# Performance work log

Measured on AMD Instinct MI355X. Metric: run time of the kernel, lower is better.

## Reference

```python
import jax, jax.numpy as jnp
import numpy as np

NUM_HEADS = 8
EPS = 1e-12  # tf.nn.l2_normalize epsilon


def _l2_normalize(t):
    # tf.nn.l2_normalize: x * rsqrt(max(sum(x^2), eps)) along last axis
    sq = jnp.sum(t * t, axis=-1, keepdims=True)
    return t * jax.lax.rsqrt(jnp.maximum(sq, EPS))


def setup_inputs() -> dict:
    key = jax.random.key(0)
    ks = jax.random.split(key, 4)
    B, N, C = 8, 4096, 512
    x = jax.random.normal(ks[0], (B, N, C), dtype=jnp.float32)
    w_qkv = jax.random.normal(ks[1], (C, 3 * C), dtype=jnp.float32) * (C ** -0.5)
    b_qkv = jnp.zeros((3 * C,), dtype=jnp.float32)
    w_proj = jax.random.normal(ks[2], (C, C), dtype=jnp.float32) * (C ** -0.5)
    b_proj = jnp.zeros((C,), dtype=jnp.float32)
    return {"x": x, "w_qkv": w_qkv, "b_qkv": b_qkv, "w_proj": w_proj, "b_proj": b_proj}


def reference(x, w_qkv, b_qkv, w_proj, b_proj):
    B, N, C = x.shape
    h = NUM_HEADS
    d = C // h
    scale = d ** -0.5
    qkv = x @ w_qkv + b_qkv                        # [B,N,3C]
    qkv = qkv.reshape(B, N, 3, h, d)
    qkv = jnp.transpose(qkv, (2, 0, 3, 1, 4))      # [3,B,h,N,d]
    q, k, v = qkv[0], qkv[1], qkv[2]
    q = _l2_normalize(q) * scale
    k = _l2_normalize(k)
    # channel-wise attention: q^T k over tokens -> [B,h,d,d]
    attn = jnp.einsum('bhnd,bhne->bhde', q, k)
    attn = jax.nn.softmax(attn, axis=-1)
    out = jnp.einsum('bhnd,bhde->bhne', v, attn)   # [B,h,N,d]
    out = jnp.transpose(out, (0, 2, 1, 3)).reshape(B, N, C)
    out = out @ w_proj + b_proj
    return out
```

## Files before the change

kernel.cpp:

```cpp
#include <hip/hip_runtime.h>
#include <stdint.h>

#define NB 8
#define NN 4096
#define NC 512
#define NH 8

typedef __bf16 bf16x8 __attribute__((ext_vector_type(8)));
typedef float floatx4 __attribute__((ext_vector_type(4)));

__device__ __forceinline__ unsigned short f2bf(float f) {
  union { float f; unsigned u; } v; v.f = f;
  return (unsigned short)((v.u + 0x7fffu + ((v.u >> 16) & 1u)) >> 16);
}
__device__ __forceinline__ float bf2f(unsigned short s) {
  union { unsigned u; float f; } v; v.u = ((unsigned)s) << 16;
  return v.f;
}
__device__ __forceinline__ float2 bfp2f(unsigned u) {
  union { unsigned x; float f; } lo, hi;
  lo.x = u << 16; hi.x = u & 0xffff0000u;
  return make_float2(lo.f, hi.f);
}

__device__ __forceinline__ void async_ld16(void* lds, const void* g) {
  auto* gp = (const __attribute__((address_space(1))) unsigned int*)(uintptr_t)g;
  auto* lp = (__attribute__((address_space(3))) unsigned int*)(uintptr_t)lds;
  __builtin_amdgcn_global_load_lds(gp, lp, 16, 0, 0);
}

__global__ __launch_bounds__(256) void k_convert(const float* __restrict__ src,
                                                 unsigned short* __restrict__ dst, int n) {
  int i = (blockIdx.x * 256 + threadIdx.x) * 4;
  if (i >= n) return;
  float4 v = *(const float4*)(src + i);
  ushort4 o;
  o.x = f2bf(v.x); o.y = f2bf(v.y); o.z = f2bf(v.z); o.w = f2bf(v.w);
  *(ushort4*)(dst + i) = o;
}

__global__ __launch_bounds__(256) void k_transpose_cvt(const float* __restrict__ w,
                                                       unsigned short* __restrict__ wt) {
  __shared__ float tile[64][65];
  int nn0 = blockIdx.x * 64, kk0 = blockIdx.y * 64;
  int t = threadIdx.x;
#pragma unroll
  for (int i = 0; i < 16; i++) {
    int id = t + i * 256;
    int r = id >> 6, c = id & 63;
    tile[c][r] = w[(size_t)(kk0 + r) * 1536 + nn0 + c];
  }
  __syncthreads();
#pragma unroll
  for (int i = 0; i < 16; i++) {
    int id = t + i * 256;
    int rn = id >> 6, ck = id & 63;
    wt[(size_t)(nn0 + rn) * 512 + kk0 + ck] = f2bf(tile[rn][ck]);
  }
}

__global__ __launch_bounds__(256) void k_gemm_qkv(const unsigned short* __restrict__ A,
                                                  const unsigned short* __restrict__ Bt,
                                                  const float* __restrict__ bias,
                                                  unsigned short* __restrict__ Cq) {
  const int K = 512, LDA = 512, LDB = 512, LDC = 1536;
  int m0 = blockIdx.x * 128, n0 = blockIdx.y * 128;
  int tid = threadIdx.x;
  int lane = tid & 63, w = tid >> 6;
  int wm = (w & 1) * 64, wn = (w >> 1) * 64;
  int quad = lane >> 4, rr = lane & 15;
  int r8 = lane >> 3, cg = lane & 7;
  int cgs = cg ^ r8;
  const int swz = rr & 7;

  __shared__ __align__(16) unsigned short Als[128][64];
  __shared__ __align__(16) unsigned short Bls[128][64];

  floatx4 acc[4][4];
#pragma unroll
  for (int i = 0; i < 4; i++)
#pragma unroll
    for (int j = 0; j < 4; j++) acc[i][j] = (floatx4){0.f, 0.f, 0.f, 0.f};

  for (int k0 = 0; k0 < K; k0 += 64) {
#pragma unroll
    for (int i = 0; i < 4; i++) {
      int row = i * 32 + w * 8 + r8;
      async_ld16(&Als[i * 32 + w * 8][0], A + (size_t)(m0 + row) * LDA + k0 + cgs * 8);
      async_ld16(&Bls[i * 32 + w * 8][0], Bt + (size_t)(n0 + row) * LDB + k0 + cgs * 8);
    }
    __syncthreads();
#pragma unroll
    for (int kk = 0; kk < 64; kk += 32) {
      int gb = kk >> 3;
      bf16x8 af[4], bfr[4];
#pragma unroll
      for (int mi = 0; mi < 4; mi++)
        af[mi] = *(const bf16x8*)&Als[wm + mi * 16 + rr][(((gb + quad) ^ swz)) * 8];
#pragma unroll
      for (int ni = 0; ni < 4; ni++)
        bfr[ni] = *(const bf16x8*)&Bls[wn + ni * 16 + rr][(((gb + quad) ^ swz)) * 8];
#pragma unroll
      for (int mi = 0; mi < 4; mi++)
#pragma unroll
        for (int ni = 0; ni < 4; ni++)
          acc[mi][ni] = __builtin_amdgcn_mfma_f32_16x16x32_bf16(af[mi], bfr[ni], acc[mi][ni], 0, 0, 0);
    }
    __syncthreads();
  }
#pragma unroll
  for (int ni = 0; ni < 4; ni++) {
    int col = n0 + wn + ni * 16 + rr;
    float bv = bias[col];
#pragma unroll
    for (int mi = 0; mi < 4; mi++) {
      int rbase = m0 + wm + mi * 16 + quad * 4;
#pragma unroll
      for (int r = 0; r < 4; r++)
        Cq[(size_t)(rbase + r) * LDC + col] = f2bf(acc[mi][ni][r] + bv);
    }
  }
}

__global__ __launch_bounds__(256) void k_attn(const unsigned short* __restrict__ QKV,
                                              float* __restrict__ logits_p) {
  int chunk = blockIdx.x, hh = blockIdx.y, b = blockIdx.z;
  int tid = threadIdx.x, w = tid >> 6, l = tid & 63;
  int quad = l >> 4, rr = l & 15;

  __shared__ __align__(16) unsigned char smem[65536];
  unsigned short* qT = (unsigned short*)smem + w * 5120;
  unsigned short* kT = qT + 2560;
  float* ps = (float*)smem;

  floatx4 acc[4][4];
#pragma unroll
  for (int i = 0; i < 4; i++)
#pragma unroll
    for (int j = 0; j < 4; j++) acc[i][j] = (floatx4){0.f, 0.f, 0.f, 0.f};

  int tok8 = l >> 3;
  int seg = l & 7;
  int sw = seg & 3;

  for (int s = 0; s < 4; s++) {
    int nbase = chunk * 512 + w * 128 + s * 32;
#pragma unroll
    for (int c = 0; c < 4; c++) {
      int n = nbase + c * 8 + tok8;
      const unsigned short* p = QKV + (size_t)(b * 4096 + n) * 1536 + hh * 64 + seg * 8;
      uint4 vq = *(const uint4*)p;
      uint4 vk = *(const uint4*)(p + 512);
      unsigned uq[4] = {vq.x, vq.y, vq.z, vq.w};
      unsigned uk[4] = {vk.x, vk.y, vk.z, vk.w};
      float qf[8], kf[8], sq = 0.f, sk = 0.f;
#pragma unroll
      for (int e = 0; e < 4; e++) {
        float2 f = bfp2f(uq[e]); qf[2 * e] = f.x; qf[2 * e + 1] = f.y; sq += f.x * f.x + f.y * f.y;
        float2 g = bfp2f(uk[e]); kf[2 * e] = g.x; kf[2 * e + 1] = g.y; sk += g.x * g.x + g.y * g.y;
      }
      sq += __shfl_xor(sq, 1); sq += __shfl_xor(sq, 2); sq += __shfl_xor(sq, 4);
      sk += __shfl_xor(sk, 1); sk += __shfl_xor(sk, 2); sk += __shfl_xor(sk, 4);
      float scq = 0.125f * rsqrtf(fmaxf(sq, 1e-12f));
      float sck = rsqrtf(fmaxf(sk, 1e-12f));
      int col = ((c ^ sw) << 3) + tok8;
#pragma unroll
      for (int j = 0; j < 8; j++) {
        int dim = seg * 8 + j;
        qT[dim * 40 + col] = f2bf(qf[j] * scq);
        kT[dim * 40 + col] = f2bf(kf[j] * sck);
      }
    }
    bf16x8 af[4], bfr[4];
#pragma unroll
    for (int mi = 0; mi < 4; mi++) {
      int s3 = (mi * 2 + (rr >> 3)) & 3;
      int off = (mi * 16 + rr) * 40 + ((quad ^ s3) << 3);
      af[mi] = *(const bf16x8*)(qT + off);
      bfr[mi] = *(const bf16x8*)(kT + off);
    }
#pragma unroll
    for (int mi = 0; mi < 4; mi++)
#pragma unroll
      for (int ni = 0; ni < 4; ni++)
        acc[mi][ni] = __builtin_amdgcn_mfma_f32_16x16x32_bf16(af[mi], bfr[ni], acc[mi][ni], 0, 0, 0);
  }

  __syncthreads();
#pragma unroll
  for (int mi = 0; mi < 4; mi++)
#pragma unroll
    for (int ni = 0; ni < 4; ni++)
#pragma unroll
      for (int r = 0; r < 4; r++) {
        int d = mi * 16 + quad * 4 + r, e = ni * 16 + rr;
        ps[w * 4096 + d * 64 + e] = acc[mi][ni][r];
      }
  __syncthreads();
  float* outp = logits_p + ((size_t)(b * 8 + hh) * 8 + chunk) * 4096;
  for (int i = tid; i < 4096; i += 256)
    outp[i] = ps[i] + ps[4096 + i] + ps[8192 + i] + ps[12288 + i];
}

__global__ __launch_bounds__(256) void k_softmax_m(const float* __restrict__ logits_p,
                                                   const float* __restrict__ wproj,
                                                   unsigned short* __restrict__ Mt) {
  int cc = blockIdx.x, hh = blockIdx.y, b = blockIdx.z;
  int t = threadIdx.x;
  __shared__ float ls[64][64];
  __shared__ float red[64][4];
  __shared__ float inv[64];
  const float* lp = logits_p + (size_t)((b * 8 + hh) * 8) * 4096;
#pragma unroll
  for (int i = 0; i < 16; i++) {
    int id = t + i * 256;
    float s = 0.f;
#pragma unroll
    for (int c = 0; c < 8; c++) s += lp[c * 4096 + id];
    ls[id >> 6][id & 63] = s;
  }
  __syncthreads();
  int row = t >> 2, part = t & 3;
  float mx = -1e30f;
#pragma unroll
  for (int j = 0; j < 16; j++) mx = fmaxf(mx, ls[row][part * 16 + j]);
  red[row][part] = mx;
  __syncthreads();
  if (part == 0) inv[row] = fmaxf(fmaxf(red[row][0], red[row][1]), fmaxf(red[row][2], red[row][3]));
  __syncthreads();
  float rm = inv[row];
  float s = 0.f;
#pragma unroll
  for (int j = 0; j < 16; j++) {
    float e = __expf(ls[row][part * 16 + j] - rm);
    ls[row][part * 16 + j] = e;
    s += e;
  }
  red[row][part] = s;
  __syncthreads();
  if (part == 0) inv[row] = 1.0f / (red[row][0] + red[row][1] + red[row][2] + red[row][3]);
  __syncthreads();

  int cout = cc * 128 + (t & 127);
  int half = t >> 7;
  float wreg[64];
#pragma unroll
  for (int ee = 0; ee < 64; ee++) wreg[ee] = wproj[(size_t)(hh * 64 + ee) * 512 + cout];
  unsigned short ob[32];
#pragma unroll
  for (int d2 = 0; d2 < 32; d2++) {
    int dd = half * 32 + d2;
    float a = 0.f;
#pragma unroll
    for (int e4 = 0; e4 < 16; e4++) {
      float4 p4 = *(const float4*)&ls[dd][e4 * 4];
      a += p4.x * wreg[e4 * 4] + p4.y * wreg[e4 * 4 + 1] + p4.z * wreg[e4 * 4 + 2] + p4.w * wreg[e4 * 4 + 3];
    }
    ob[d2] = f2bf(a * inv[dd]);
  }
  uint4* dst = (uint4*)(Mt + ((size_t)(b * 512 + cout)) * 512 + hh * 64 + half * 32);
#pragma unroll
  for (int i = 0; i < 4; i++) dst[i] = ((const uint4*)ob)[i];
}

__global__ __launch_bounds__(256) void k_gemm_out(const unsigned short* __restrict__ QKV,
                                                  const unsigned short* __restrict__ MtAll,
                                                  const float* __restrict__ bias,
                                                  float* __restrict__ Out) {
  const int K = 512, LDA = 1536, LDB = 512, LDC = 512;
  int b = blockIdx.x >> 5;
  int m0 = (blockIdx.x & 31) * 128;
  int n0 = blockIdx.y * 128;
  const unsigned short* A = QKV + (size_t)b * NN * 1536 + 1024;
  const unsigned short* Bt = MtAll + (size_t)b * 512 * 512;
  int tid = threadIdx.x;
  int lane = tid & 63, w = tid >> 6;
  int wm = (w & 1) * 64, wn = (w >> 1) * 64;
  int quad = lane >> 4, rr = lane & 15;
  int r8 = lane >> 3, cg = lane & 7;
  int cgs = cg ^ r8;
  const int swz = rr & 7;

  __shared__ __align__(16) unsigned short Als[128][64];
  __shared__ __align__(16) unsigned short Bls[128][64];

  floatx4 acc[4][4];
#pragma unroll
  for (int i = 0; i < 4; i++)
#pragma unroll
    for (int j = 0; j < 4; j++) acc[i][j] = (floatx4){0.f, 0.f, 0.f, 0.f};

  for (int k0 = 0; k0 < K; k0 += 64) {
#pragma unroll
    for (int i = 0; i < 4; i++) {
      int row = i * 32 + w * 8 + r8;
      async_ld16(&Als[i * 32 + w * 8][0], A + (size_t)(m0 + row) * LDA + k0 + cgs * 8);
      async_ld16(&Bls[i * 32 + w * 8][0], Bt + (size_t)(n0 + row) * LDB + k0 + cgs * 8);
    }
    __syncthreads();
#pragma unroll
    for (int kk = 0; kk < 64; kk += 32) {
      int gb = kk >> 3;
      bf16x8 af[4], bfr[4];
#pragma unroll
      for (int mi = 0; mi < 4; mi++)
        af[mi] = *(const bf16x8*)&Als[wm + mi * 16 + rr][(((gb + quad) ^ swz)) * 8];
#pragma unroll
      for (int ni = 0; ni < 4; ni++)
        bfr[ni] = *(const bf16x8*)&Bls[wn + ni * 16 + rr][(((gb + quad) ^ swz)) * 8];
#pragma unroll
      for (int mi = 0; mi < 4; mi++)
#pragma unroll
        for (int ni = 0; ni < 4; ni++)
          acc[mi][ni] = __builtin_amdgcn_mfma_f32_16x16x32_bf16(af[mi], bfr[ni], acc[mi][ni], 0, 0, 0);
    }
    __syncthreads();
  }
#pragma unroll
  for (int ni = 0; ni < 4; ni++) {
    int col = n0 + wn + ni * 16 + rr;
    float bv = bias[col];
#pragma unroll
    for (int mi = 0; mi < 4; mi++) {
      int rbase = m0 + wm + mi * 16 + quad * 4;
#pragma unroll
      for (int r = 0; r < 4; r++)
        Out[(size_t)b * NN * LDC + (size_t)(rbase + r) * LDC + col] = acc[mi][ni][r] + bv;
    }
  }
}

extern "C" void kernel_launch(void* const* d_in, const int* in_sizes, int n_in,
                              void* d_out, int out_size, void* d_ws, size_t ws_size,
                              hipStream_t stream) {
  const float* x      = (const float*)d_in[0];
  const float* w_qkv  = (const float*)d_in[1];
  const float* b_qkv  = (const float*)d_in[2];
  const float* w_proj = (const float*)d_in[3];
  const float* b_proj = (const float*)d_in[4];
  float* out = (float*)d_out;

  char* ws = (char*)d_ws;
  size_t off = 0;
  auto alloc = [&](size_t bytes) -> void* {
    void* p = ws + off;
    off += (bytes + 255) & ~(size_t)255;
    return p;
  };
  unsigned short* xb       = (unsigned short*)alloc((size_t)NB * NN * NC * 2);
  unsigned short* wT       = (unsigned short*)alloc((size_t)1536 * 512 * 2);
  unsigned short* qkvb     = (unsigned short*)alloc((size_t)NB * NN * 3 * NC * 2);
  float*          logits_p = (float*)alloc((size_t)NB * NH * 8 * 4096 * 4);
  unsigned short* Mt       = (unsigned short*)alloc((size_t)NB * 512 * 512 * 2);

  k_convert<<<16384, 256, 0, stream>>>(x, xb, NB * NN * NC);
  k_transpose_cvt<<<dim3(24, 8), 256, 0, stream>>>(w_qkv, wT);
  k_gemm_qkv<<<dim3(256, 12), 256, 0, stream>>>(xb, wT, b_qkv, qkvb);
  k_attn<<<dim3(8, 8, 8), 256, 0, stream>>>(qkvb, logits_p);
  k_softmax_m<<<dim3(4, 8, 8), 256, 0, stream>>>(logits_p, w_proj, Mt);
  k_gemm_out<<<dim3(256, 4), 256, 0, stream>>>(qkvb, Mt, b_proj, out);
}
```

Baseline: 276.5 us.

## Fuse prep kernels, XCD-aware GEMM block mapping, split attention into more chunks

Merges the x conversion and weight transpose into one launch, saving a kernel launch. Remaps the QKV and output GEMM block indices so that blocks sharing an M-row stripe land on the same XCD, which is meant to improve L2 reuse. Doubles the attention token chunks to 16 and reduces per-block shared memory to raise occupancy. It also serializes the per-wave accumulation in LDS and doubles the softmax blocks by splitting rows. The trade-off is more partial logits to sum in softmax and extra barriers.

New measurement: 268.1 us. 3.0% less time.

```diff
diff --git a/kernel.cpp b/kernel.cpp
--- a/kernel.cpp
+++ b/kernel.cpp
@@ -5,6 +5,7 @@
 #define NN 4096
 #define NC 512
 #define NH 8
+#define ATTN_CH 16
 
 typedef __bf16 bf16x8 __attribute__((ext_vector_type(8)));
 typedef float floatx4 __attribute__((ext_vector_type(4)));
@@ -12,10 +13,6 @@
 __device__ __forceinline__ unsigned short f2bf(float f) {
   union { float f; unsigned u; } v; v.f = f;
   return (unsigned short)((v.u + 0x7fffu + ((v.u >> 16) & 1u)) >> 16);
-}
-__device__ __forceinline__ float bf2f(unsigned short s) {
-  union { unsigned u; float f; } v; v.u = ((unsigned)s) << 16;
-  return v.f;
 }
 __device__ __forceinline__ float2 bfp2f(unsigned u) {
   union { unsigned x; float f; } lo, hi;
@@ -29,20 +26,22 @@
   __builtin_amdgcn_global_load_lds(gp, lp, 16, 0, 0);
 }
 
-__global__ __launch_bounds__(256) void k_convert(const float* __restrict__ src,
-                                                 unsigned short* __restrict__ dst, int n) {
-  int i = (blockIdx.x * 256 + threadIdx.x) * 4;
-  if (i >= n) return;
-  float4 v = *(const float4*)(src + i);
-  ushort4 o;
-  o.x = f2bf(v.x); o.y = f2bf(v.y); o.z = f2bf(v.z); o.w = f2bf(v.w);
-  *(ushort4*)(dst + i) = o;
-}
-
-__global__ __launch_bounds__(256) void k_transpose_cvt(const float* __restrict__ w,
-                                                       unsigned short* __restrict__ wt) {
+__global__ __launch_bounds__(256) void k_prep(const float* __restrict__ x,
+                                              unsigned short* __restrict__ xb,
+                                              const float* __restrict__ w,
+                                              unsigned short* __restrict__ wt) {
+  int bid = blockIdx.x;
+  if (bid < 16384) {
+    int i = (bid * 256 + threadIdx.x) * 4;
+    float4 v = *(const float4*)(x + i);
+    ushort4 o;
+    o.x = f2bf(v.x); o.y = f2bf(v.y); o.z = f2bf(v.z); o.w = f2bf(v.w);
+    *(ushort4*)(xb + i) = o;
+    return;
+  }
   __shared__ float tile[64][65];
-  int nn0 = blockIdx.x * 64, kk0 = blockIdx.y * 64;
+  int b2 = bid - 16384;
+  int nn0 = (b2 % 24) * 64, kk0 = (b2 / 24) * 64;
   int t = threadIdx.x;
 #pragma unroll
   for (int i = 0; i < 16; i++) {
@@ -64,7 +63,11 @@
                                                   const float* __restrict__ bias,
                                                   unsigned short* __restrict__ Cq) {
   const int K = 512, LDA = 512, LDB = 512, LDC = 1536;
-  int m0 = blockIdx.x * 128, n0 = blockIdx.y * 128;
+  int bid = blockIdx.x;
+  int xcd = bid & 7, local = bid >> 3;
+  int mloc = local / 12, nt = local - mloc * 12;
+  int m0 = (xcd * 32 + mloc) * 128, n0 = nt * 128;
+
   int tid = threadIdx.x;
   int lane = tid & 63, w = tid >> 6;
   int wm = (w & 1) * 64, wn = (w >> 1) * 64;
@@ -128,7 +131,7 @@
   int tid = threadIdx.x, w = tid >> 6, l = tid & 63;
   int quad = l >> 4, rr = l & 15;
 
-  __shared__ __align__(16) unsigned char smem[65536];
+  __shared__ __align__(16) unsigned char smem[40960];
   unsigned short* qT = (unsigned short*)smem + w * 5120;
   unsigned short* kT = qT + 2560;
   float* ps = (float*)smem;
@@ -143,8 +146,8 @@
   int seg = l & 7;
   int sw = seg & 3;
 
-  for (int s = 0; s < 4; s++) {
-    int nbase = chunk * 512 + w * 128 + s * 32;
+  for (int s = 0; s < 2; s++) {
+    int nbase = chunk * 256 + w * 64 + s * 32;
 #pragma unroll
     for (int c = 0; c < 4; c++) {
       int n = nbase + c * 8 + tok8;
@@ -187,58 +190,73 @@
   }
 
   __syncthreads();
-#pragma unroll
-  for (int mi = 0; mi < 4; mi++)
-#pragma unroll
-    for (int ni = 0; ni < 4; ni++)
-#pragma unroll
-      for (int r = 0; r < 4; r++) {
-        int d = mi * 16 + quad * 4 + r, e = ni * 16 + rr;
-        ps[w * 4096 + d * 64 + e] = acc[mi][ni][r];
-      }
-  __syncthreads();
-  float* outp = logits_p + ((size_t)(b * 8 + hh) * 8 + chunk) * 4096;
-  for (int i = tid; i < 4096; i += 256)
-    outp[i] = ps[i] + ps[4096 + i] + ps[8192 + i] + ps[12288 + i];
+  for (int r2 = 0; r2 < 4; r2++) {
+    if (w == r2) {
+#pragma unroll
+      for (int mi = 0; mi < 4; mi++)
+#pragma unroll
+        for (int ni = 0; ni < 4; ni++)
+#pragma unroll
+          for (int r = 0; r < 4; r++) {
+            int d = mi * 16 + quad * 4 + r, e = ni * 16 + rr;
+            if (r2 == 0) ps[d * 64 + e] = acc[mi][ni][r];
+            else         ps[d * 64 + e] += acc[mi][ni][r];
+          }
+    }
+    __syncthreads();
+  }
+  float* outp = logits_p + ((size_t)(b * 8 + hh) * ATTN_CH + chunk) * 4096;
+  for (int i = tid; i < 4096; i += 256) outp[i] = ps[i];
 }
 
 __global__ __launch_bounds__(256) void k_softmax_m(const float* __restrict__ logits_p,
                                                    const float* __restrict__ wproj,
                                                    unsigned short* __restrict__ Mt) {
-  int cc = blockIdx.x, hh = blockIdx.y, b = blockIdx.z;
+  int cc = blockIdx.x & 3, rh = blockIdx.x >> 2;
+  int hh = blockIdx.y, b = blockIdx.z;
   int t = threadIdx.x;
-  __shared__ float ls[64][64];
-  __shared__ float red[64][4];
-  __shared__ float inv[64];
-  const float* lp = logits_p + (size_t)((b * 8 + hh) * 8) * 4096;
-#pragma unroll
-  for (int i = 0; i < 16; i++) {
+  __shared__ float ls[32][64];
+  __shared__ float red[32][8];
+  __shared__ float inv[32];
+  const float* lp = logits_p + (size_t)((b * 8 + hh) * ATTN_CH) * 4096 + rh * 2048;
+#pragma unroll
+  for (int i = 0; i < 8; i++) {
     int id = t + i * 256;
     float s = 0.f;
 #pragma unroll
-    for (int c = 0; c < 8; c++) s += lp[c * 4096 + id];
+    for (int c = 0; c < ATTN_CH; c++) s += lp[c * 4096 + id];
     ls[id >> 6][id & 63] = s;
   }
   __syncthreads();
-  int row = t >> 2, part = t & 3;
+  int row = t >> 3, part = t & 7;
   float mx = -1e30f;
 #pragma unroll
-  for (int j = 0; j < 16; j++) mx = fmaxf(mx, ls[row][part * 16 + j]);
+  for (int j = 0; j < 8; j++) mx = fmaxf(mx, ls[row][part * 8 + j]);
   red[row][part] = mx;
   __syncthreads();
-  if (part == 0) inv[row] = fmaxf(fmaxf(red[row][0], red[row][1]), fmaxf(red[row][2], red[row][3]));
+  if (part == 0) {
+    float m2 = red[row][0];
+#pragma unroll
+    for (int j = 1; j < 8; j++) m2 = fmaxf(m2, red[row][j]);
+    inv[row] = m2;
+  }
   __syncthreads();
   float rm = inv[row];
   float s = 0.f;
 #pragma unroll
-  for (int j = 0; j < 16; j++) {
-    float e = __expf(ls[row][part * 16 + j] - rm);
-    ls[row][part * 16 + j] = e;
+  for (int j = 0; j < 8; j++) {
+    float e = __expf(ls[row][part * 8 + j] - rm);
+    ls[row][part * 8 + j] = e;
     s += e;
   }
   red[row][part] = s;
   __syncthreads();
-  if (part == 0) inv[row] = 1.0f / (red[row][0] + red[row][1] + red[row][2] + red[row][3]);
+  if (part == 0) {
+    float s2 = 0.f;
+#pragma unroll
+    for (int j = 0; j < 8; j++) s2 += red[row][j];
+    inv[row] = 1.0f / s2;
+  }
   __syncthreads();
 
   int cout = cc * 128 + (t & 127);
@@ -246,10 +264,10 @@
   float wreg[64];
 #pragma unroll
   for (int ee = 0; ee < 64; ee++) wreg[ee] = wproj[(size_t)(hh * 64 + ee) * 512 + cout];
-  unsigned short ob[32];
-#pragma unroll
-  for (int d2 = 0; d2 < 32; d2++) {
-    int dd = half * 32 + d2;
+  unsigned short ob[16];
+#pragma unroll
+  for (int d2 = 0; d2 < 16; d2++) {
+    int dd = half * 16 + d2;
     float a = 0.f;
 #pragma unroll
     for (int e4 = 0; e4 < 16; e4++) {
@@ -258,9 +276,9 @@
     }
     ob[d2] = f2bf(a * inv[dd]);
   }
-  uint4* dst = (uint4*)(Mt + ((size_t)(b * 512 + cout)) * 512 + hh * 64 + half * 32);
-#pragma unroll
-  for (int i = 0; i < 4; i++) dst[i] = ((const uint4*)ob)[i];
+  uint4* dst = (uint4*)(Mt + ((size_t)(b * 512 + cout)) * 512 + hh * 64 + rh * 32 + half * 16);
+  dst[0] = ((const uint4*)ob)[0];
+  dst[1] = ((const uint4*)ob)[1];
 }
 
 __global__ __launch_bounds__(256) void k_gemm_out(const unsigned short* __restrict__ QKV,
@@ -268,9 +286,13 @@
                                                   const float* __restrict__ bias,
                                                   float* __restrict__ Out) {
   const int K = 512, LDA = 1536, LDB = 512, LDC = 512;
-  int b = blockIdx.x >> 5;
-  int m0 = (blockIdx.x & 31) * 128;
-  int n0 = blockIdx.y * 128;
+  int bid = blockIdx.x;
+  int xcd = bid & 7, local = bid >> 3;
+  int mloc = local >> 2, nt = local & 3;
+  int g = xcd * 32 + mloc;
+  int b = g >> 5;
+  int m0 = (g & 31) * 128;
+  int n0 = nt * 128;
   const unsigned short* A = QKV + (size_t)b * NN * 1536 + 1024;
   const unsigned short* Bt = MtAll + (size_t)b * 512 * 512;
   int tid = threadIdx.x;
@@ -350,13 +372,12 @@
   unsigned short* xb       = (unsigned short*)alloc((size_t)NB * NN * NC * 2);
   unsigned short* wT       = (unsigned short*)alloc((size_t)1536 * 512 * 2);
   unsigned short* qkvb     = (unsigned short*)alloc((size_t)NB * NN * 3 * NC * 2);
-  float*          logits_p = (float*)alloc((size_t)NB * NH * 8 * 4096 * 4);
+  float*          logits_p = (float*)alloc((size_t)NB * NH * ATTN_CH * 4096 * 4);
   unsigned short* Mt       = (unsigned short*)alloc((size_t)NB * 512 * 512 * 2);
 
-  k_convert<<<16384, 256, 0, stream>>>(x, xb, NB * NN * NC);
-  k_transpose_cvt<<<dim3(24, 8), 256, 0, stream>>>(w_qkv, wT);
-  k_gemm_qkv<<<dim3(256, 12), 256, 0, stream>>>(xb, wT, b_qkv, qkvb);
-  k_attn<<<dim3(8, 8, 8), 256, 0, stream>>>(qkvb, logits_p);
-  k_softmax_m<<<dim3(4, 8, 8), 256, 0, stream>>>(logits_p, w_proj, Mt);
-  k_gemm_out<<<dim3(256, 4), 256, 0, stream>>>(qkvb, Mt, b_proj, out);
-}
+  k_prep<<<16576, 256, 0, stream>>>(x, xb, w_qkv, wT);
+  k_gemm_qkv<<<3072, 256, 0, stream>>>(xb, wT, b_qkv, qkvb);
+  k_attn<<<dim3(ATTN_CH, 8, 8), 256, 0, stream>>>(qkvb, logits_p);
+  k_softmax_m<<<dim3(8, 8, 8), 256, 0, stream>>>(logits_p, w_proj, Mt);
+  k_gemm_out<<<1024, 256, 0, stream>>>(qkvb, Mt, b_proj, out);
+}
```
